# Optimization experiments

Measured on AMD Instinct MI355X. Metric: run time of the kernel, lower is better.

The kernel has to match this reference:

```python
import jax, jax.numpy as jnp
import numpy as np

H = 4                 # num_heads
GATE_NORM = 16.0      # gate_logit_normalizer
EPS = 1e-5            # RMSNorm eps


def setup_inputs() -> dict:
    key = jax.random.key(0)
    ks = jax.random.split(key, 12)
    B, T, D = 8, 4096, 1024
    Dk_total, Dv_total, Dlow = D // 2, D, 16

    def w(k, shape, fan_in):
        return jax.random.normal(k, shape, dtype=jnp.float32) * (fan_in ** -0.5)

    return {
        "x": jax.random.normal(ks[0], (B, T, D), dtype=jnp.float32),
        "Wq": w(ks[1], (D, Dk_total), D),
        "Wk": w(ks[2], (D, Dk_total), D),
        "Wv": w(ks[3], (D, Dv_total), D),
        "gk_w1": w(ks[4], (D, Dlow), D),
        "gk_w2": w(ks[5], (Dlow, Dk_total), Dlow),
        "gk_b2": jnp.zeros((Dk_total,), dtype=jnp.float32),
        "Wg": w(ks[6], (D, Dv_total), D),
        "g_norm_w": jnp.ones((Dv_total // H,), dtype=jnp.float32),
        "Wo": w(ks[7], (Dv_total, D), Dv_total),
    }


def _gla_forward(x, Wq, Wk, Wv, gk_w1, gk_w2, gk_b2, Wg, g_norm_w, Wo):
    B, T, D = x.shape
    Dk = Wq.shape[1] // H
    Dv = Wv.shape[1] // H

    q = (x @ Wq).reshape(B, T, H, Dk) * (Dk ** -0.5)
    k = (x @ Wk).reshape(B, T, H, Dk)
    v = (x @ Wv).reshape(B, T, H, Dv)
    # low-rank gate logits -> log-space decay gk (<= 0)
    gk = jax.nn.log_sigmoid((x @ gk_w1) @ gk_w2 + gk_b2) / GATE_NORM
    gk = gk.reshape(B, T, H, Dk)

    # recurrent gated linear attention:
    #   S_t = exp(gk_t)[:, None] * S_{t-1} + k_t^T v_t ;  o_t = q_t @ S_t
    def step(S, qkvg):
        qt, kt, vt, gt = qkvg          # each [B, H, Dk|Dv]
        S = jnp.exp(gt)[..., None] * S + kt[..., None] * vt[..., None, :]
        ot = jnp.einsum("bhk,bhkv->bhv", qt, S)
        return S, ot

    S0 = jnp.zeros((B, H, Dk, Dv), dtype=x.dtype)
    tm = lambda a: jnp.swapaxes(a, 0, 1)  # [B,T,...] -> [T,B,...]
    _, o = jax.lax.scan(step, S0, (tm(q), tm(k), tm(v), tm(gk)))
    o = jnp.swapaxes(o, 0, 1)            # [B, T, H, Dv]

    # output gate: RMSNorm(o) * swish(g), per head
    g = (x @ Wg).reshape(B, T, H, Dv)
    o = o * jax.lax.rsqrt(jnp.mean(o * o, axis=-1, keepdims=True) + EPS) * g_norm_w
    o = o * (g * jax.nn.sigmoid(g))
    return o.reshape(B, T, H * Dv) @ Wo


def reference(x, Wq, Wk, Wv, gk_w1, gk_w2, gk_b2, Wg, g_norm_w, Wo):
    return _gla_forward(x, Wq, Wk, Wv, gk_w1, gk_w2, gk_b2, Wg, g_norm_w, Wo)
```

## Files before the change

kernel.cpp:

```cpp
#include <hip/hip_runtime.h>
#include <hip/hip_bf16.h>
#include <cstdint>
#include <cstddef>

typedef __hip_bfloat16 bf16;
typedef __attribute__((ext_vector_type(8))) short short8;
typedef __attribute__((ext_vector_type(4))) float floatx4;

__device__ __forceinline__ void gload_lds16(const void* g, void* l) {
  __builtin_amdgcn_global_load_lds(
      (__attribute__((address_space(1))) void*)(uintptr_t)g,
      (__attribute__((address_space(3))) void*)l, 16, 0, 0);
}

__device__ __forceinline__ short f2bbits(float f) {
  bf16 h = __float2bfloat16(f);
  return __builtin_bit_cast(short, h);
}
__device__ __forceinline__ float b2f(short s) {
  return __bfloat162float(__builtin_bit_cast(bf16, s));
}

__global__ __launch_bounds__(256) void convert_x(const float* __restrict__ x,
                                                 bf16* __restrict__ xb) {
  size_t i = ((size_t)blockIdx.x * 256 + threadIdx.x) * 8;
  float4 f0 = *(const float4*)(x + i);
  float4 f1 = *(const float4*)(x + i + 4);
  short8 r;
  r[0] = f2bbits(f0.x); r[1] = f2bbits(f0.y); r[2] = f2bbits(f0.z); r[3] = f2bbits(f0.w);
  r[4] = f2bbits(f1.x); r[5] = f2bbits(f1.y); r[6] = f2bbits(f1.z); r[7] = f2bbits(f1.w);
  *(short8*)(xb + i) = r;
}

__global__ __launch_bounds__(256) void transpose_w(const float* __restrict__ src,
                                                   bf16* __restrict__ dst, int cols) {
  __shared__ float tile[32][33];
  int n0 = blockIdx.x * 32, k0 = blockIdx.y * 32;
  int tx = threadIdx.x & 31, ty = threadIdx.x >> 5;
#pragma unroll
  for (int i = 0; i < 32; i += 8) {
    int kk = k0 + ty + i, nn = n0 + tx;
    tile[ty + i][tx] = (nn < cols) ? src[(size_t)kk * cols + nn] : 0.0f;
  }
  __syncthreads();
#pragma unroll
  for (int i = 0; i < 32; i += 8) {
    int nn = n0 + ty + i, kk = k0 + tx;
    if (nn < cols) dst[(size_t)nn * 1024 + kk] = __float2bfloat16(tile[tx][ty + i]);
  }
}

#define BARR __builtin_amdgcn_s_barrier()
#define WAITV(n) asm volatile("s_waitcnt vmcnt(" #n ")" ::: "memory")

#define STA(buf, h, tau) do { \
  gload_lds16(pA + (size_t)(h) * K64 + (size_t)(tau) * 64, \
              &lds[(buf) * 16384 + (h) * 8192 + w * 512]); \
  gload_lds16(pA + K128 + (size_t)(h) * K64 + (size_t)(tau) * 64, \
              &lds[(buf) * 16384 + (h) * 8192 + 4096 + w * 512]); \
} while (0)

#define STB(buf, h, tau) do { \
  gload_lds16(pB + (size_t)(h) * K32 + (size_t)(tau) * 64, \
              &lds[32768 + (buf) * 16384 + (h) * 8192 + w * 512]); \
  gload_lds16(pB + K128 + (size_t)(h) * K32 + (size_t)(tau) * 64, \
              &lds[32768 + (buf) * 16384 + (h) * 8192 + 4096 + w * 512]); \
} while (0)

#define LDA(mh, buf) do { \
  _Pragma("unroll") \
  for (int mp = 0; mp < 4; ++mp) { \
    const short* p_ = &lds[(buf) * 16384 + (mh) * 8192 + aRow + mp * 1024]; \
    a[mp][0] = *(const short8*)(p_ + g0); \
    a[mp][1] = *(const short8*)(p_ + g1); \
  } \
} while (0)

#define LDB(nh, buf, d0, d1) do { \
  const short* p_ = &lds[(buf) * 16384 + (nh) * 8192 + bRow]; \
  d0[0] = *(const short8*)(p_ + g0); \
  d0[1] = *(const short8*)(p_ + g1); \
  d1[0] = *(const short8*)(p_ + 1024 + g0); \
  d1[1] = *(const short8*)(p_ + 1024 + g1); \
} while (0)

#define MQ(MB, NB, d0, d1) do { \
  __builtin_amdgcn_s_setprio(1); \
  _Pragma("unroll") \
  for (int mp = 0; mp < 4; ++mp) { \
    acc[(MB) + mp][(NB)] = __builtin_amdgcn_mfma_f32_16x16x32_bf16(a[mp][0], d0[0], acc[(MB) + mp][(NB)], 0, 0, 0); \
    acc[(MB) + mp][(NB)] = __builtin_amdgcn_mfma_f32_16x16x32_bf16(a[mp][1], d0[1], acc[(MB) + mp][(NB)], 0, 0, 0); \
    acc[(MB) + mp][(NB) + 1] = __builtin_amdgcn_mfma_f32_16x16x32_bf16(a[mp][0], d1[0], acc[(MB) + mp][(NB) + 1], 0, 0, 0); \
    acc[(MB) + mp][(NB) + 1] = __builtin_amdgcn_mfma_f32_16x16x32_bf16(a[mp][1], d1[1], acc[(MB) + mp][(NB) + 1], 0, 0, 0); \
  } \
  __builtin_amdgcn_s_setprio(0); \
} while (0)

__global__ __launch_bounds__(512, 2) void gemm256(
    const bf16* __restrict__ A, const bf16* __restrict__ Bt, const int K,
    const int nTN, const int mode,
    bf16* __restrict__ oq, bf16* __restrict__ okk, bf16* __restrict__ ov,
    bf16* __restrict__ ogg, float* __restrict__ oo) {
  extern __shared__ __align__(16) short lds[];
  const int tid = threadIdx.x;
  const int w = tid >> 6, lane = tid & 63;
  const int wr = w >> 2, wc = w & 3;
  const int l15 = lane & 15, lq = lane >> 4;
  const int e7 = lane & 7, l3 = lane >> 3;
  const int gAp = (lane & 7) ^ l3;

  const int cpx = (int)gridDim.x >> 3;
  const int bid = blockIdx.x;
  const int swz = (bid & 7) * cpx + (bid >> 3);
  const int mt = swz / nTN, nt = swz - mt * nTN;
  const int m0 = mt << 8, n0 = nt << 8;

  const size_t K64 = (size_t)K * 64, K128 = (size_t)K * 128, K32 = (size_t)K * 32;
  const bf16* pA = A + (size_t)(m0 + w * 8 + l3) * K + gAp * 8;
  const bf16* pB = Bt + (size_t)(n0 + (w >> 2) * 64 + (w & 3) * 8 + l3) * K + gAp * 8;

  const int g0 = ((lq ^ e7) & 7) * 8;
  const int g1 = (((lq + 4) ^ e7) & 7) * 8;
  const int aRow = (wr * 64 + l15) * 64;
  const int bRow = 32768 + (wc * 32 + l15) * 64;

  floatx4 acc[8][4] = {};
  short8 a[4][2], bb0[2], bb1[2], bb2[2], bb3[2];

  STA(0, 0, 0); STB(0, 0, 0); STB(0, 1, 0); STA(0, 1, 0);
  STA(1, 0, 1); STB(1, 1, 1);
  WAITV(4);
  BARR;

  const int nIter = K >> 7;
  for (int t = 0; t < nIter; ++t) {
    const bool nl = (t < nIter - 1);
    const int t1 = 2 * t + 1, t2 = 2 * t + 2, t3 = 2 * t + 3;
    LDA(0, 0); LDB(0, 0, bb0, bb1);
    STA(1, 1, t1);
    BARR; MQ(0, 0, bb0, bb1); BARR;
    LDB(1, 0, bb2, bb3);
    STB(1, 0, t1);
    BARR; MQ(0, 2, bb2, bb3); BARR;
    LDA(1, 0);
    if (nl) STA(0, 0, t2);
    BARR; MQ(4, 2, bb2, bb3); BARR;
    LDB(0, 0, bb0, bb1);
    if (nl) STB(0, 1, t2);
    BARR; MQ(4, 0, bb0, bb1);
    if (nl) { WAITV(4); } else { WAITV(0); }
    BARR;
    LDA(0, 1); LDB(0, 1, bb0, bb1);
    if (nl) STA(0, 1, t2);
    BARR; MQ(0, 0, bb0, bb1); BARR;
    LDB(1, 1, bb2, bb3);
    if (nl) STB(0, 0, t2);
    BARR; MQ(0, 2, bb2, bb3); BARR;
    LDA(1, 1);
    if (nl) STA(1, 0, t3);
    BARR; MQ(4, 2, bb2, bb3); BARR;
    LDB(0, 1, bb0, bb1);
    if (nl) STB(1, 1, t3);
    BARR; MQ(4, 0, bb0, bb1);
    if (nl) { WAITV(4); }
    BARR;
  }

  const int rq = lq * 4;
#pragma unroll
  for (int m = 0; m < 8; ++m) {
#pragma unroll
    for (int n = 0; n < 4; ++n) {
      const int col = n0 + wc * 64 + n * 16 + l15;
#pragma unroll
      for (int r = 0; r < 4; ++r) {
        const size_t row = (size_t)(m0 + wr * 128 + m * 16 + rq + r);
        const float val = acc[m][n][r];
        if (mode == 1) {
          oo[row * 1024 + col] = val;
        } else if (col < 512) {
          oq[row * 512 + col] = __float2bfloat16(val * 0.08838834764831845f);
        } else if (col < 1024) {
          okk[row * 512 + (col - 512)] = __float2bfloat16(val);
        } else if (col < 2048) {
          ov[row * 1024 + (col - 1024)] = __float2bfloat16(val);
        } else {
          ogg[row * 1024 + (col - 2048)] = __float2bfloat16(val);
        }
      }
    }
  }
}

__global__ __launch_bounds__(256) void gate_decay2(const float* __restrict__ x,
                                                   const float* __restrict__ w1,
                                                   const float* __restrict__ w2,
                                                   const float* __restrict__ b2,
                                                   float* __restrict__ gkout) {
  __shared__ float sp[256];
  __shared__ float sz[16];
  const int m0 = blockIdx.x * 4, tid = threadIdx.x;
  const int j = tid & 15, dpart = tid >> 4;
  float w1r[64];
#pragma unroll
  for (int e = 0; e < 64; ++e) w1r[e] = w1[(dpart * 64 + e) * 16 + j];
  float w2r[32];
#pragma unroll
  for (int jj = 0; jj < 16; ++jj) {
    w2r[jj] = w2[jj * 512 + tid];
    w2r[16 + jj] = w2[jj * 512 + tid + 256];
  }
  const float b2a = b2[tid], b2b = b2[tid + 256];
  for (int r = 0; r < 4; ++r) {
    const int m = m0 + r;
    const float* xr = x + (size_t)m * 1024 + dpart * 64;
    float acc = 0.f;
#pragma unroll
    for (int e = 0; e < 64; ++e) acc = fmaf(xr[e], w1r[e], acc);
    sp[tid] = acc;
    __syncthreads();
    if (tid < 16) {
      float s = 0.f;
#pragma unroll
      for (int p = 0; p < 16; ++p) s += sp[p * 16 + tid];
      sz[tid] = s;
    }
    __syncthreads();
    float t = b2a;
#pragma unroll
    for (int jj = 0; jj < 16; ++jj) t = fmaf(sz[jj], w2r[jj], t);
    const float ls = fminf(t, 0.f) - log1pf(__expf(-fabsf(t)));
    gkout[(size_t)m * 512 + tid] = ls * 0.0625f;
    float t2 = b2b;
#pragma unroll
    for (int jj = 0; jj < 16; ++jj) t2 = fmaf(sz[jj], w2r[16 + jj], t2);
    const float ls2 = fminf(t2, 0.f) - log1pf(__expf(-fabsf(t2)));
    gkout[(size_t)m * 512 + tid + 256] = ls2 * 0.0625f;
    if (r < 3) __syncthreads();
  }
}

__global__ __launch_bounds__(128) void chunk_prep(
    const bf16* __restrict__ q, const bf16* __restrict__ k,
    const float* __restrict__ gk, bf16* __restrict__ qt,
    bf16* __restrict__ kt, float* __restrict__ dtot) {
  const int cid = blockIdx.x;
  const int c = cid & 63, h = (cid >> 6) & 3, b = cid >> 8;
  const int d = threadIdx.x;
  const size_t rowbase = ((size_t)(b * 4096 + c * 64)) * 512 + h * 128 + d;
  const size_t obase = (size_t)cid * 8192 + d;
  float bsum = 0.f;
  for (int i = 0; i < 64; ++i) {
    const size_t src = rowbase + (size_t)i * 512;
    bsum += gk[src];
    qt[obase + (size_t)i * 128] = __float2bfloat16(__bfloat162float(q[src]) * __expf(bsum));
    kt[obase + (size_t)i * 128] = __float2bfloat16(__bfloat162float(k[src]) * __expf(-bsum));
  }
  dtot[cid * 128 + d] = __expf(bsum);
}

__global__ __launch_bounds__(256) void chunk_intra(
    const bf16* __restrict__ qt, const bf16* __restrict__ kt,
    const float* __restrict__ dtot, const bf16* __restrict__ v,
    bf16* __restrict__ oi, bf16* __restrict__ ut) {
  __shared__ __align__(16) short lA[64 * 72];
  __shared__ __align__(16) short stg[27648];
  short* sQ = stg;
  short* sK = stg + 8704;
  short* sVT = stg;
  short* sKhT = stg + 18432;
  const int cid = blockIdx.x;
  const int c = cid & 63, h = (cid >> 6) & 3, b = cid >> 8;
  const int tid = threadIdx.x, wv = tid >> 6, lane = tid & 63;
  const int l15 = lane & 15, q8 = (lane >> 4) * 8, rq = (lane >> 4) * 4;

  {
    const int row = tid >> 2, seg = (tid & 3) * 32;
    const size_t src = (size_t)cid * 8192 + row * 128 + seg;
    const short8* qs = (const short8*)(qt + src);
    const short8* ks = (const short8*)(kt + src);
    short8* qd = (short8*)&sQ[row * 136 + seg];
    short8* kd = (short8*)&sK[row * 136 + seg];
#pragma unroll
    for (int t = 0; t < 4; ++t) { qd[t] = qs[t]; kd[t] = ks[t]; }
  }
  __syncthreads();
  {
    short8 af[4];
#pragma unroll
    for (int kf = 0; kf < 4; ++kf)
      af[kf] = *(const short8*)&sQ[(wv * 16 + l15) * 136 + kf * 32 + q8];
#pragma unroll
    for (int nt = 0; nt < 4; ++nt) {
      floatx4 accA = {0.f, 0.f, 0.f, 0.f};
#pragma unroll
      for (int kf = 0; kf < 4; ++kf) {
        short8 bfr = *(const short8*)&sK[(nt * 16 + l15) * 136 + kf * 32 + q8];
        accA = __builtin_amdgcn_mfma_f32_16x16x32_bf16(af[kf], bfr, accA, 0, 0, 0);
      }
#pragma unroll
      for (int r = 0; r < 4; ++r) {
        const int i = wv * 16 + rq + r, jj = nt * 16 + l15;
        lA[i * 72 + jj] = f2bbits(jj <= i ? accA[r] : 0.f);
      }
    }
  }
  __syncthreads();
  {
#pragma unroll
    for (int e = 0; e < 8; ++e) {
      const int idx = tid + e * 256;
      const int jj = idx >> 5, n0 = (idx & 31) * 8;
      short8 vv = *(const short8*)(v + ((size_t)(b * 4096 + c * 64 + jj)) * 1024 + h * 256 + n0);
#pragma unroll
      for (int t = 0; t < 8; ++t) sVT[(n0 + t) * 72 + jj] = vv[t];
    }
#pragma unroll
    for (int e = 0; e < 4; ++e) {
      const int idx = tid + e * 256;
      const int jj = idx >> 4, d0 = (idx & 15) * 8;
      short8 kk = *(const short8*)(kt + (size_t)cid * 8192 + jj * 128 + d0);
#pragma unroll
      for (int t = 0; t < 8; ++t)
        sKhT[(d0 + t) * 72 + jj] = f2bbits(b2f(kk[t]) * dtot[cid * 128 + d0 + t]);
    }
  }
  __syncthreads();
  {
    short8 aA0 = *(const short8*)&lA[(wv * 16 + l15) * 72 + q8];
    short8 aA1 = *(const short8*)&lA[(wv * 16 + l15) * 72 + 32 + q8];
#pragma unroll
    for (int nt = 0; nt < 16; ++nt) {
      short8 b0 = *(const short8*)&sVT[(nt * 16 + l15) * 72 + q8];
      short8 b1 = *(const short8*)&sVT[(nt * 16 + l15) * 72 + 32 + q8];
      floatx4 acc = {0.f, 0.f, 0.f, 0.f};
      acc = __builtin_amdgcn_mfma_f32_16x16x32_bf16(aA0, b0, acc, 0, 0, 0);
      acc = __builtin_amdgcn_mfma_f32_16x16x32_bf16(aA1, b1, acc, 0, 0, 0);
#pragma unroll
      for (int r = 0; r < 4; ++r) {
        const int i = wv * 16 + rq + r;
        oi[(size_t)cid * 16384 + i * 256 + nt * 16 + l15] = __builtin_bit_cast(bf16, f2bbits(acc[r]));
      }
    }
  }
  {
    short8 aV[4][2];
#pragma unroll
    for (int mt = 0; mt < 4; ++mt) {
      aV[mt][0] = *(const short8*)&sVT[(wv * 64 + mt * 16 + l15) * 72 + q8];
      aV[mt][1] = *(const short8*)&sVT[(wv * 64 + mt * 16 + l15) * 72 + 32 + q8];
    }
#pragma unroll
    for (int nt = 0; nt < 8; ++nt) {
      short8 b0 = *(const short8*)&sKhT[(nt * 16 + l15) * 72 + q8];
      short8 b1 = *(const short8*)&sKhT[(nt * 16 + l15) * 72 + 32 + q8];
#pragma unroll
      for (int mt = 0; mt < 4; ++mt) {
        floatx4 acc = {0.f, 0.f, 0.f, 0.f};
        acc = __builtin_amdgcn_mfma_f32_16x16x32_bf16(aV[mt][0], b0, acc, 0, 0, 0);
        acc = __builtin_amdgcn_mfma_f32_16x16x32_bf16(aV[mt][1], b1, acc, 0, 0, 0);
#pragma unroll
        for (int r = 0; r < 4; ++r) {
          const int vr = wv * 64 + mt * 16 + rq + r;
          ut[(size_t)cid * 32768 + vr * 128 + nt * 16 + l15] = __builtin_bit_cast(bf16, f2bbits(acc[r]));
        }
      }
    }
  }
}

__global__ __launch_bounds__(256) void state_prop(
    bf16* __restrict__ su,
    const float* __restrict__ dtot) {
  const int ng = blockIdx.x, h = blockIdx.y, b = blockIdx.z;
  const int tid = threadIdx.x;
  const int nrow = ng * 16 + (tid >> 4), kseg = (tid & 15) * 8;
  const int cid0 = (b * 4 + h) * 64;
  size_t a = (size_t)cid0 * 32768 + (size_t)nrow * 128 + kseg;
  float S[8];
#pragma unroll
  for (int e = 0; e < 8; ++e) S[e] = 0.f;
  short8 u0 = *(const short8*)(su + a);
  for (int c = 0; c < 64; ++c) {
    short8 un0;
    if (c < 63) un0 = *(const short8*)(su + a + 32768);
    const float4 d0 = *(const float4*)(dtot + (cid0 + c) * 128 + kseg);
    const float4 d1 = *(const float4*)(dtot + (cid0 + c) * 128 + kseg + 4);
    short8 s0;
#pragma unroll
    for (int e = 0; e < 8; ++e) s0[e] = f2bbits(S[e]);
    *(short8*)(su + a) = s0;
    const float dd[8] = {d0.x, d0.y, d0.z, d0.w, d1.x, d1.y, d1.z, d1.w};
#pragma unroll
    for (int e = 0; e < 8; ++e) S[e] = fmaf(dd[e], S[e], b2f(u0[e]));
    u0 = un0;
    a += 32768;
  }
}

__global__ __launch_bounds__(256, 2) void o_inter_norm(
    const bf16* __restrict__ qt, const bf16* __restrict__ scb,
    const bf16* __restrict__ oi, const bf16* __restrict__ g,
    const float* __restrict__ gnw, bf16* __restrict__ og) {
  __shared__ __align__(16) short sQ[64 * 136];
  __shared__ float sp[64 * 4];
  const int cid = blockIdx.x;
  const int c = cid & 63, h = (cid >> 6) & 3, b = cid >> 8;
  const int tid = threadIdx.x, wv = tid >> 6, lane = tid & 63;
  const int l15 = lane & 15, q8 = (lane >> 4) * 8, rq = (lane >> 4) * 4;
  {
    const int row = tid >> 2, seg = (tid & 3) * 32;
    const short8* qs = (const short8*)(qt + (size_t)cid * 8192 + row * 128 + seg);
    short8* qd = (short8*)&sQ[row * 136 + seg];
#pragma unroll
    for (int t = 0; t < 4; ++t) qd[t] = qs[t];
  }
  __syncthreads();
  short8 af[4][4];
#pragma unroll
  for (int i = 0; i < 4; ++i)
#pragma unroll
    for (int kf = 0; kf < 4; ++kf)
      af[i][kf] = *(const short8*)&sQ[(i * 16 + l15) * 136 + kf * 32 + q8];
  floatx4 acc[4][4] = {};
#pragma unroll
  for (int j = 0; j < 4; ++j) {
#pragma unroll
    for (int kf = 0; kf < 4; ++kf) {
      short8 bfr = *(const short8*)(scb + (size_t)cid * 32768 +
                                    (size_t)(wv * 64 + j * 16 + l15) * 128 + kf * 32 + q8);
#pragma unroll
      for (int i = 0; i < 4; ++i)
        acc[i][j] = __builtin_amdgcn_mfma_f32_16x16x32_bf16(af[i][kf], bfr, acc[i][j], 0, 0, 0);
    }
  }
#pragma unroll
  for (int i = 0; i < 4; ++i) {
#pragma unroll
    for (int r = 0; r < 4; ++r) {
      const int row = i * 16 + rq + r;
      float p = 0.f;
#pragma unroll
      for (int j = 0; j < 4; ++j) {
        const int col = wv * 64 + j * 16 + l15;
        const float v = acc[i][j][r] +
            __bfloat162float(oi[(size_t)cid * 16384 + row * 256 + col]);
        acc[i][j][r] = v;
        p = fmaf(v, v, p);
      }
      p += __shfl_xor(p, 1); p += __shfl_xor(p, 2);
      p += __shfl_xor(p, 4); p += __shfl_xor(p, 8);
      if (l15 == 0) sp[row * 4 + wv] = p;
    }
  }
  __syncthreads();
  const size_t rowg0 = (size_t)(b * 4096 + c * 64);
#pragma unroll
  for (int i = 0; i < 4; ++i) {
#pragma unroll
    for (int r = 0; r < 4; ++r) {
      const int row = i * 16 + rq + r;
      const float ms = (sp[row * 4] + sp[row * 4 + 1] + sp[row * 4 + 2] + sp[row * 4 + 3]) *
                       (1.0f / 256.0f);
      const float sc = rsqrtf(ms + 1e-5f);
#pragma unroll
      for (int j = 0; j < 4; ++j) {
        const int col = wv * 64 + j * 16 + l15;
        const size_t gi = (rowg0 + row) * 1024 + h * 256 + col;
        const float gv = __bfloat162float(g[gi]);
        const float sw = gv * (1.0f / (1.0f + __expf(-gv)));
        og[gi] = __float2bfloat16(acc[i][j][r] * sc * gnw[col] * sw);
      }
    }
  }
}

extern "C" void kernel_launch(void* const* d_in, const int* in_sizes, int n_in,
                              void* d_out, int out_size, void* d_ws, size_t ws_size,
                              hipStream_t stream) {
  const float* x   = (const float*)d_in[0];
  const float* Wq  = (const float*)d_in[1];
  const float* Wk  = (const float*)d_in[2];
  const float* Wv  = (const float*)d_in[3];
  const float* gw1 = (const float*)d_in[4];
  const float* gw2 = (const float*)d_in[5];
  const float* gb2 = (const float*)d_in[6];
  const float* Wg  = (const float*)d_in[7];
  const float* gnw = (const float*)d_in[8];
  const float* Wo  = (const float*)d_in[9];
  float* out = (float*)d_out;

  static bool attr_set = false;
  if (!attr_set) {
    hipFuncSetAttribute(reinterpret_cast<const void*>(gemm256),
                        hipFuncAttributeMaxDynamicSharedMemorySize, 131072);
    attr_set = true;
  }

  const size_t Mi = 1048576;
  uint8_t* w = (uint8_t*)d_ws;
  bf16*  wallT = (bf16*)(w);
  bf16*  woT   = (bf16*)(w + 6 * Mi);
  float* dtot  = (float*)(w + 8 * Mi);
  bf16*  xb    = (bf16*)(w + 9 * Mi);
  bf16*  qt    = (bf16*)(w + 9 * Mi);
  bf16*  ktb   = (bf16*)(w + 41 * Mi);
  float* qbF   = (float*)(w + 73 * Mi);
  bf16*  qb    = (bf16*)(w + 73 * Mi);
  bf16*  kb    = (bf16*)(w + 137 * Mi);
  bf16*  utb   = (bf16*)(w + 73 * Mi);
  float* gkb   = (float*)(w + 201 * Mi);
  bf16*  oib   = (bf16*)(w + 201 * Mi);
  bf16*  vb    = (bf16*)(w + 265 * Mi);
  bf16*  ogat  = (bf16*)(w + 265 * Mi);
  bf16*  gb    = (bf16*)(w + 329 * Mi);
  (void)qbF;

  convert_x<<<dim3(16384), 256, 0, stream>>>(x, xb);
  transpose_w<<<dim3(16, 32), 256, 0, stream>>>(Wq, wallT, 512);
  transpose_w<<<dim3(16, 32), 256, 0, stream>>>(Wk, wallT + (size_t)512 * 1024, 512);
  transpose_w<<<dim3(32, 32), 256, 0, stream>>>(Wv, wallT + (size_t)1024 * 1024, 1024);
  transpose_w<<<dim3(32, 32), 256, 0, stream>>>(Wg, wallT + (size_t)2048 * 1024, 1024);
  transpose_w<<<dim3(32, 32), 256, 0, stream>>>(Wo, woT, 1024);
  gemm256<<<dim3(1536), 512, 131072, stream>>>(xb, wallT, 1024, 12, 0, qb, kb, vb, gb, nullptr);
  gate_decay2<<<dim3(8192), 256, 0, stream>>>(x, gw1, gw2, gb2, gkb);
  chunk_prep<<<dim3(2048), 128, 0, stream>>>(qb, kb, gkb, qt, ktb, dtot);
  chunk_intra<<<dim3(2048), 256, 0, stream>>>(qt, ktb, dtot, vb, oib, utb);
  state_prop<<<dim3(16, 4, 8), 256, 0, stream>>>(utb, dtot);
  o_inter_norm<<<dim3(2048), 256, 0, stream>>>(qt, utb, oib, gb, gnw, ogat);
  gemm256<<<dim3(512), 512, 131072, stream>>>(ogat, woT, 1024, 4, 1, nullptr, nullptr, nullptr, nullptr, out);
}
```

Measured before the change: 1.015 ms.

## Single-buffer GEMM mainloop with higher occupancy and fuse x conversion into gate kernel

The 256x256 GEMM drops its double-buffered, interleaved load/compute schedule for a single-buffered loop: each K=64 step computes from LDS, then all threads barrier, issue the next tile's loads and wait for them. LDS drops to 64KB and launch bounds rise to 4 blocks per CU, so occupancy is meant to hide latency in place of software pipelining. Separately, the fp32-to-bf16 conversion of x moves into the gate-decay kernel, which already reads x, removing one kernel launch and one full read of x. The GEMM change risks exposing global load latency, since loads no longer overlap with MFMA work within a block.

```diff
diff --git a/kernel.cpp b/kernel.cpp
--- a/kernel.cpp
+++ b/kernel.cpp
@@ -19,17 +19,6 @@
 }
 __device__ __forceinline__ float b2f(short s) {
   return __bfloat162float(__builtin_bit_cast(bf16, s));
-}
-
-__global__ __launch_bounds__(256) void convert_x(const float* __restrict__ x,
-                                                 bf16* __restrict__ xb) {
-  size_t i = ((size_t)blockIdx.x * 256 + threadIdx.x) * 8;
-  float4 f0 = *(const float4*)(x + i);
-  float4 f1 = *(const float4*)(x + i + 4);
-  short8 r;
-  r[0] = f2bbits(f0.x); r[1] = f2bbits(f0.y); r[2] = f2bbits(f0.z); r[3] = f2bbits(f0.w);
-  r[4] = f2bbits(f1.x); r[5] = f2bbits(f1.y); r[6] = f2bbits(f1.z); r[7] = f2bbits(f1.w);
-  *(short8*)(xb + i) = r;
 }
 
 __global__ __launch_bounds__(256) void transpose_w(const float* __restrict__ src,
@@ -53,31 +42,31 @@
 #define BARR __builtin_amdgcn_s_barrier()
 #define WAITV(n) asm volatile("s_waitcnt vmcnt(" #n ")" ::: "memory")
 
-#define STA(buf, h, tau) do { \
+#define STA(h, tau) do { \
   gload_lds16(pA + (size_t)(h) * K64 + (size_t)(tau) * 64, \
-              &lds[(buf) * 16384 + (h) * 8192 + w * 512]); \
+              &lds[(h) * 8192 + w * 512]); \
   gload_lds16(pA + K128 + (size_t)(h) * K64 + (size_t)(tau) * 64, \
-              &lds[(buf) * 16384 + (h) * 8192 + 4096 + w * 512]); \
+              &lds[(h) * 8192 + 4096 + w * 512]); \
 } while (0)
 
-#define STB(buf, h, tau) do { \
+#define STB(h, tau) do { \
   gload_lds16(pB + (size_t)(h) * K32 + (size_t)(tau) * 64, \
-              &lds[32768 + (buf) * 16384 + (h) * 8192 + w * 512]); \
+              &lds[16384 + (h) * 8192 + w * 512]); \
   gload_lds16(pB + K128 + (size_t)(h) * K32 + (size_t)(tau) * 64, \
-              &lds[32768 + (buf) * 16384 + (h) * 8192 + 4096 + w * 512]); \
+              &lds[16384 + (h) * 8192 + 4096 + w * 512]); \
 } while (0)
 
-#define LDA(mh, buf) do { \
+#define LDA(mh) do { \
   _Pragma("unroll") \
   for (int mp = 0; mp < 4; ++mp) { \
-    const short* p_ = &lds[(buf) * 16384 + (mh) * 8192 + aRow + mp * 1024]; \
+    const short* p_ = &lds[(mh) * 8192 + aRow + mp * 1024]; \
     a[mp][0] = *(const short8*)(p_ + g0); \
     a[mp][1] = *(const short8*)(p_ + g1); \
   } \
 } while (0)
 
-#define LDB(nh, buf, d0, d1) do { \
-  const short* p_ = &lds[(buf) * 16384 + (nh) * 8192 + bRow]; \
+#define LDB(nh, d0, d1) do { \
+  const short* p_ = &lds[16384 + (nh) * 8192 + bRow]; \
   d0[0] = *(const short8*)(p_ + g0); \
   d0[1] = *(const short8*)(p_ + g1); \
   d1[0] = *(const short8*)(p_ + 1024 + g0); \
@@ -96,7 +85,7 @@
   __builtin_amdgcn_s_setprio(0); \
 } while (0)
 
-__global__ __launch_bounds__(512, 2) void gemm256(
+__global__ __launch_bounds__(512, 4) void gemm256(
     const bf16* __restrict__ A, const bf16* __restrict__ Bt, const int K,
     const int nTN, const int mode,
     bf16* __restrict__ oq, bf16* __restrict__ okk, bf16* __restrict__ ov,
@@ -122,47 +111,29 @@
   const int g0 = ((lq ^ e7) & 7) * 8;
   const int g1 = (((lq + 4) ^ e7) & 7) * 8;
   const int aRow = (wr * 64 + l15) * 64;
-  const int bRow = 32768 + (wc * 32 + l15) * 64;
+  const int bRow = (wc * 32 + l15) * 64;
 
   floatx4 acc[8][4] = {};
   short8 a[4][2], bb0[2], bb1[2], bb2[2], bb3[2];
 
-  STA(0, 0, 0); STB(0, 0, 0); STB(0, 1, 0); STA(0, 1, 0);
-  STA(1, 0, 1); STB(1, 1, 1);
-  WAITV(4);
+  STA(0, 0); STB(0, 0); STA(1, 0); STB(1, 0);
+  WAITV(0);
   BARR;
 
-  const int nIter = K >> 7;
+  const int nIter = K >> 6;
   for (int t = 0; t < nIter; ++t) {
-    const bool nl = (t < nIter - 1);
-    const int t1 = 2 * t + 1, t2 = 2 * t + 2, t3 = 2 * t + 3;
-    LDA(0, 0); LDB(0, 0, bb0, bb1);
-    STA(1, 1, t1);
-    BARR; MQ(0, 0, bb0, bb1); BARR;
-    LDB(1, 0, bb2, bb3);
-    STB(1, 0, t1);
-    BARR; MQ(0, 2, bb2, bb3); BARR;
-    LDA(1, 0);
-    if (nl) STA(0, 0, t2);
-    BARR; MQ(4, 2, bb2, bb3); BARR;
-    LDB(0, 0, bb0, bb1);
-    if (nl) STB(0, 1, t2);
-    BARR; MQ(4, 0, bb0, bb1);
-    if (nl) { WAITV(4); } else { WAITV(0); }
+    LDA(0); LDB(0, bb0, bb1);
+    MQ(0, 0, bb0, bb1);
+    LDB(1, bb2, bb3);
+    MQ(0, 2, bb2, bb3);
+    LDA(1);
+    MQ(4, 2, bb2, bb3);
+    MQ(4, 0, bb0, bb1);
     BARR;
-    LDA(0, 1); LDB(0, 1, bb0, bb1);
-    if (nl) STA(0, 1, t2);
-    BARR; MQ(0, 0, bb0, bb1); BARR;
-    LDB(1, 1, bb2, bb3);
-    if (nl) STB(0, 0, t2);
-    BARR; MQ(0, 2, bb2, bb3); BARR;
-    LDA(1, 1);
-    if (nl) STA(1, 0, t3);
-    BARR; MQ(4, 2, bb2, bb3); BARR;
-    LDB(0, 1, bb0, bb1);
-    if (nl) STB(1, 1, t3);
-    BARR; MQ(4, 0, bb0, bb1);
-    if (nl) { WAITV(4); }
+    if (t < nIter - 1) {
+      STA(0, t + 1); STB(0, t + 1); STA(1, t + 1); STB(1, t + 1);
+      WAITV(0);
+    }
     BARR;
   }
 
@@ -192,15 +163,30 @@
   }
 }
 
-__global__ __launch_bounds__(256) void gate_decay2(const float* __restrict__ x,
-                                                   const float* __restrict__ w1,
-                                                   const float* __restrict__ w2,
-                                                   const float* __restrict__ b2,
-                                                   float* __restrict__ gkout) {
+__global__ __launch_bounds__(256) void convert_gate(const float* __restrict__ x,
+                                                    const float* __restrict__ w1,
+                                                    const float* __restrict__ w2,
+                                                    const float* __restrict__ b2,
+                                                    bf16* __restrict__ xb,
+                                                    float* __restrict__ gkout) {
   __shared__ float sp[256];
   __shared__ float sz[16];
   const int m0 = blockIdx.x * 4, tid = threadIdx.x;
   const int j = tid & 15, dpart = tid >> 4;
+  {
+    const float* xrow = x + (size_t)m0 * 1024;
+    bf16* xbrow = xb + (size_t)m0 * 1024;
+#pragma unroll
+    for (int u = 0; u < 2; ++u) {
+      const size_t off = (size_t)(tid + u * 256) * 8;
+      float4 f0 = *(const float4*)(xrow + off);
+      float4 f1 = *(const float4*)(xrow + off + 4);
+      short8 rr;
+      rr[0] = f2bbits(f0.x); rr[1] = f2bbits(f0.y); rr[2] = f2bbits(f0.z); rr[3] = f2bbits(f0.w);
+      rr[4] = f2bbits(f1.x); rr[5] = f2bbits(f1.y); rr[6] = f2bbits(f1.z); rr[7] = f2bbits(f1.w);
+      *(short8*)(xbrow + off) = rr;
+    }
+  }
   float w1r[64];
 #pragma unroll
   for (int e = 0; e < 64; ++e) w1r[e] = w1[(dpart * 64 + e) * 16 + j];
@@ -493,7 +479,7 @@
   static bool attr_set = false;
   if (!attr_set) {
     hipFuncSetAttribute(reinterpret_cast<const void*>(gemm256),
-                        hipFuncAttributeMaxDynamicSharedMemorySize, 131072);
+                        hipFuncAttributeMaxDynamicSharedMemorySize, 65536);
     attr_set = true;
   }
 
@@ -505,7 +491,6 @@
   bf16*  xb    = (bf16*)(w + 9 * Mi);
   bf16*  qt    = (bf16*)(w + 9 * Mi);
   bf16*  ktb   = (bf16*)(w + 41 * Mi);
-  float* qbF   = (float*)(w + 73 * Mi);
   bf16*  qb    = (bf16*)(w + 73 * Mi);
   bf16*  kb    = (bf16*)(w + 137 * Mi);
   bf16*  utb   = (bf16*)(w + 73 * Mi);
@@ -514,19 +499,17 @@
   bf16*  vb    = (bf16*)(w + 265 * Mi);
   bf16*  ogat  = (bf16*)(w + 265 * Mi);
   bf16*  gb    = (bf16*)(w + 329 * Mi);
-  (void)qbF;
-
-  convert_x<<<dim3(16384), 256, 0, stream>>>(x, xb);
+
+  convert_gate<<<dim3(8192), 256, 0, stream>>>(x, gw1, gw2, gb2, xb, gkb);
   transpose_w<<<dim3(16, 32), 256, 0, stream>>>(Wq, wallT, 512);
   transpose_w<<<dim3(16, 32), 256, 0, stream>>>(Wk, wallT + (size_t)512 * 1024, 512);
   transpose_w<<<dim3(32, 32), 256, 0, stream>>>(Wv, wallT + (size_t)1024 * 1024, 1024);
   transpose_w<<<dim3(32, 32), 256, 0, stream>>>(Wg, wallT + (size_t)2048 * 1024, 1024);
   transpose_w<<<dim3(32, 32), 256, 0, stream>>>(Wo, woT, 1024);
-  gemm256<<<dim3(1536), 512, 131072, stream>>>(xb, wallT, 1024, 12, 0, qb, kb, vb, gb, nullptr);
-  gate_decay2<<<dim3(8192), 256, 0, stream>>>(x, gw1, gw2, gb2, gkb);
+  gemm256<<<dim3(1536), 512, 65536, stream>>>(xb, wallT, 1024, 12, 0, qb, kb, vb, gb, nullptr);
   chunk_prep<<<dim3(2048), 128, 0, stream>>>(qb, kb, gkb, qt, ktb, dtot);
   chunk_intra<<<dim3(2048), 256, 0, stream>>>(qt, ktb, dtot, vb, oib, utb);
   state_prop<<<dim3(16, 4, 8), 256, 0, stream>>>(utb, dtot);
   o_inter_norm<<<dim3(2048), 256, 0, stream>>>(qt, utb, oib, gb, gnw, ogat);
-  gemm256<<<dim3(512), 512, 131072, stream>>>(ogat, woT, 1024, 4, 1, nullptr, nullptr, nullptr, nullptr, out);
-}
+  gemm256<<<dim3(512), 512, 65536, stream>>>(ogat, woT, 1024, 4, 1, nullptr, nullptr, nullptr, nullptr, out);
+}
```

New measurement: 2.958 ms. 2.91x slower.
